# Kernel tuning notes

Measured on AMD Instinct MI355X. Metric: run time of the kernel, lower is better.

## Reference

```python
import jax, jax.numpy as jnp
import numpy as np

EPSILON = 1e-15
CUTOFF = 5.0
N_RBF = 16           # num_radial_filters -> RBF dim = 2*16+1 = 33
SCALE = 8            # _quadrature_points_per_atom_scaling


def poly_envelope_5_2(x):
    # e3nn.poly_envelope(5, 2): f'(x) ~ x^5 (1-x)^2, f(0)=1, f(1)=0
    x2 = x * x
    x6 = x2 * x2 * x2
    f = 1.0 - 28.0 * x6 + 48.0 * x6 * x - 21.0 * x6 * x2
    return jnp.where(x < 1.0, f, jnp.zeros_like(x))


def sin_cos_basis(r, n_rbf):
    r = r[..., None]                                  # [A,T,1]
    k = jnp.arange(1, n_rbf + 1, dtype=r.dtype)       # [n_rbf]
    return jnp.sqrt(2.0) * jnp.concatenate(
        [0.1 * jnp.ones_like(r), jnp.sin(k * jnp.pi * r), jnp.cos(k * jnp.pi * r)],
        axis=-1,
    )                                                 # [A,T,2*n_rbf+1]


def spherical_harmonics_l012_norm(d):
    # Real spherical harmonics up to l=2, e3nn m-ordering, normalization='norm'
    # (each l-block has unit norm for unit input directions).
    x, y, z = d[..., 0], d[..., 1], d[..., 2]
    r2 = x * x + y * y + z * z
    s3 = jnp.sqrt(3.0)
    one = jnp.ones_like(x)
    return jnp.stack(
        [
            one,                       # l=0
            y, z, x,                   # l=1 (m=-1,0,1)
            s3 * x * y,                # l=2 m=-2
            s3 * y * z,                # l=2 m=-1
            0.5 * (3.0 * z * z - r2),  # l=2 m=0
            s3 * x * z,                # l=2 m=1
            0.5 * s3 * (x * x - y * y) # l=2 m=2
        ],
        axis=-1,
    )                                  # [A,T,9]


def setup_inputs() -> dict:
    key = jax.random.key(0)
    k1, k2, k3, k4 = jax.random.split(key, 4)
    A, N = 64, 200000
    nuc_pos = 4.0 * jax.random.normal(k1, (A, 3), dtype=jnp.float32)
    grid_coords = 4.0 * jax.random.normal(k2, (N, 3), dtype=jnp.float32)
    weights = jax.random.uniform(k3, (N,), dtype=jnp.float32)
    n = jax.random.uniform(k4, (N,), dtype=jnp.float32)
    atom_mask = jnp.ones((A,), dtype=bool)
    return {"nuc_pos": nuc_pos, "atom_mask": atom_mask,
            "grid_coords": grid_coords, "weights": weights, "n": n}


def reference(nuc_pos, atom_mask, grid_coords, weights, n):
    g = grid_coords / CUTOFF                          # [N,3]
    p = nuc_pos / CUTOFF                              # [A,3]
    diff = p[:, None] - g[None]                       # [A,N,3]
    dist = jnp.linalg.norm(diff, axis=-1)             # [A,N]
    A, N = dist.shape
    T = min(N, SCALE * N // A)                        # static
    idx = jnp.argsort(dist, axis=1)[:, :T]            # [A,T] nearest grid points
    diff = jnp.take_along_axis(diff, idx[:, :, None], axis=1)   # [A,T,3]
    dist = jnp.take_along_axis(dist, idx, axis=1)                # [A,T]
    n_t = n[idx]                                      # [A,T]
    w_t = weights[idx]                                # [A,T]
    rbf = sin_cos_basis(dist, N_RBF) * poly_envelope_5_2(dist)[..., None]  # [A,T,33]
    dirs = diff / (dist[..., None] + EPSILON)         # [A,T,3]
    sh = spherical_harmonics_l012_norm(dirs)          # [A,T,9]
    node_feats = jnp.einsum('atr,ath,at,at->arh', rbf, sh, n_t, w_t)  # [A,33,9]
    return node_feats
```

## Files before the change

kernel.cpp:

```cpp
#include <hip/hip_runtime.h>
#include <hip/hip_fp16.h>


typedef float f32x4 __attribute__((ext_vector_type(4)));
typedef int   i32x4 __attribute__((ext_vector_type(4)));

#define SLICES 32
#define NB1    256
#define NB2    512
#define CLAMP0 4000u
#define NCHUNK SLICES
#define PBSTR  304
#define CUT25  0x41C80000u
#define WROWS  49
#define CSTR   136
#define CSTRD  (CSTR / 2)

__device__ __forceinline__ unsigned pack2h(float a, float b) {
  __half2 h = __floats2half2_rn(a, b);
  return *reinterpret_cast<unsigned*>(&h);
}

__device__ __forceinline__ unsigned pkbf(float a, float b) {
  unsigned r;
  asm("v_cvt_pk_bf16_f32 %0, %1, %2" : "=v"(r) : "v"(a), "v"(b));
  return r;
}

__device__ __forceinline__ void mfma_acc(f32x4& d, i32x4 a, i32x4 b) {
  asm("v_mfma_f32_16x16x32_bf16 %0, %1, %2, %0" : "+v"(d) : "v"(a), "v"(b));
}

__global__ __launch_bounds__(256) void enc_hist_store(
    const float* __restrict__ nuc, const float* __restrict__ grid,
    const float* __restrict__ wv, const float* __restrict__ nv, int N,
    unsigned* __restrict__ hists, unsigned* __restrict__ cnt,
    unsigned* __restrict__ bitsArr, uint2* __restrict__ pay, int scap,
    unsigned* __restrict__ ghist2) {
  __shared__ unsigned lh[4][NB1];
  __shared__ unsigned s_cnt;
  int a = blockIdx.x / SLICES, s = blockIdx.x % SLICES;
  int tid = threadIdx.x, lane = tid & 63, w = tid >> 6;
  if (tid < NB1) {
    lh[0][tid] = 0; lh[1][tid] = 0; lh[2][tid] = 0; lh[3][tid] = 0;
  }
  if (tid == 0) s_cnt = 0;
  {
    const int stripe = NB2 / SLICES;
    if (tid < stripe) ghist2[(size_t)a * NB2 + s * stripe + tid] = 0;
  }
  __syncthreads();
  unsigned* lhw = lh[w];

  float px = nuc[3*a+0], py = nuc[3*a+1], pz = nuc[3*a+2];
  unsigned* segb = bitsArr + (size_t)blockIdx.x * scap;
  uint2*    segp = pay     + (size_t)blockIdx.x * scap;
  const float4* G4 = (const float4*)grid;
  const float4* W4 = (const float4*)wv;
  const float4* V4 = (const float4*)nv;
  int nq = N >> 2;
  int qper = (nq + SLICES - 1) / SLICES;
  int qlo = s * qper, qhi = min(nq, qlo + qper);

  for (int qb = qlo; qb < qhi; qb += 256) {
    int qi = qb + tid;
    bool qv = qi < qhi;
    float dxs[4], dys[4], dzs[4], nws[4];
    unsigned bt[4];
    if (qv) {
      float4 A4 = G4[3*qi], B4 = G4[3*qi+1], C4 = G4[3*qi+2];
      float4 w4 = W4[qi], v4 = V4[qi];
      float xs[4] = {A4.x, A4.w, B4.z, C4.y};
      float ys[4] = {A4.y, B4.x, B4.w, C4.z};
      float zs[4] = {A4.z, B4.y, C4.x, C4.w};
      nws[0] = v4.x * w4.x; nws[1] = v4.y * w4.y;
      nws[2] = v4.z * w4.z; nws[3] = v4.w * w4.w;
      #pragma unroll
      for (int k = 0; k < 4; ++k) {
        float dx = px - xs[k], dy = py - ys[k], dz = pz - zs[k];
        dxs[k] = dx; dys[k] = dy; dzs[k] = dz;
        float d2 = __fmaf_rn(dx, dx, __fmaf_rn(dy, dy, __fmul_rn(dz, dz)));
        bt[k] = __float_as_uint(d2);
        if (bt[k] < CUT25) {
          int cb = (int)(bt[k] >> 18) - (int)CLAMP0;
          atomicAdd(&lhw[cb > 0 ? cb : 0], 1u);
        }
      }
    } else {
      #pragma unroll
      for (int k = 0; k < 4; ++k) bt[k] = 0xFFFFFFFFu;
    }
    unsigned csel = 0;
    #pragma unroll
    for (int k = 0; k < 4; ++k) csel += (bt[k] < CUT25) ? 1u : 0u;
    unsigned p = csel;
    #pragma unroll
    for (int d = 1; d < 64; d <<= 1) {
      unsigned t = __shfl_up(p, d);
      if (lane >= d) p += t;
    }
    unsigned wtot = __shfl(p, 63);
    unsigned excl = p - csel;
    unsigned base = 0;
    if (wtot) {
      if (lane == 0) base = atomicAdd(&s_cnt, wtot);
      base = __shfl(base, 0);
      unsigned pos = base + excl;
      #pragma unroll
      for (int k = 0; k < 4; ++k) {
        if (bt[k] < CUT25) {
          if (pos < (unsigned)scap) {
            segb[pos] = bt[k];
            segp[pos] = make_uint2(pack2h(dxs[k], dys[k]), pack2h(dzs[k], nws[k]));
          }
          ++pos;
        }
      }
    }
  }
  if (s == SLICES - 1) {
    for (int i = 4*nq + tid; i < N; i += 256) {
      float dx = px - grid[3*i+0], dy = py - grid[3*i+1], dz = pz - grid[3*i+2];
      float d2 = __fmaf_rn(dx, dx, __fmaf_rn(dy, dy, __fmul_rn(dz, dz)));
      unsigned bits = __float_as_uint(d2);
      bool sel = bits < CUT25;
      if (sel) {
        int cb = (int)(bits >> 18) - (int)CLAMP0;
        atomicAdd(&lhw[cb > 0 ? cb : 0], 1u);
      }
      unsigned long long mm = __ballot(sel);
      if (mm) {
        int leader = __ffsll(mm) - 1;
        unsigned base = 0;
        if (lane == leader) base = atomicAdd(&s_cnt, (unsigned)__popcll(mm));
        base = __shfl(base, leader);
        if (sel) {
          unsigned pos = base + (unsigned)__popcll(mm & ((1ull << lane) - 1ull));
          if (pos < (unsigned)scap) {
            segb[pos] = bits;
            segp[pos] = make_uint2(pack2h(dx, dy), pack2h(dz, nv[i] * wv[i]));
          }
        }
      }
    }
  }
  __syncthreads();
  if (tid < NB1) {
    unsigned v = lh[0][tid] + lh[1][tid] + lh[2][tid] + lh[3][tid];
    hists[(size_t)blockIdx.x * NB1 + tid] = v;
  }
  if (tid == 0) cnt[blockIdx.x] = s_cnt;
}

__global__ __launch_bounds__(256) void enc_scan1(
    const unsigned* __restrict__ hists, unsigned T,
    unsigned* __restrict__ b1r, unsigned* __restrict__ r2r) {
  __shared__ unsigned lh[NB1];
  __shared__ unsigned s_bin, s_pre;
  int a = blockIdx.x, tid = threadIdx.x;
  if (tid < NB1) {
    unsigned acc = 0;
    const unsigned* base = hists + (size_t)a * SLICES * NB1 + tid;
    #pragma unroll 8
    for (int t = 0; t < SLICES; ++t) acc += base[(size_t)t * NB1];
    lh[tid] = acc;
  }
  if (tid == 0) { s_bin = NB1 - 1; s_pre = 0; }
  __syncthreads();
  if (tid < 64) {
    int lane = tid, base = 4 * lane;
    unsigned h0 = lh[base], h1 = lh[base+1], h2 = lh[base+2], h3 = lh[base+3];
    unsigned ssum = h0 + h1 + h2 + h3;
    unsigned p = ssum;
    #pragma unroll
    for (int d = 1; d < 64; d <<= 1) {
      unsigned t = __shfl_up(p, d);
      if (lane >= d) p += t;
    }
    unsigned excl = p - ssum;
    if (excl < T && T <= p) {
      unsigned cum = excl;
      unsigned hh[4] = {h0, h1, h2, h3};
      #pragma unroll
      for (int k = 0; k < 4; ++k) {
        if (cum + hh[k] >= T) { s_bin = (unsigned)(base + k); s_pre = cum; break; }
        cum += hh[k];
      }
    }
  }
  __syncthreads();
  if (tid == 0) { b1r[a] = s_bin; r2r[a] = T - s_pre; }
}

__global__ __launch_bounds__(256) void enc_fine(
    const unsigned* __restrict__ b1r, const unsigned* __restrict__ cnt,
    const unsigned* __restrict__ bitsArr, int scap,
    unsigned* __restrict__ ghist2) {
  int seg_id = blockIdx.x;
  int a = seg_id / SLICES;
  unsigned b1c = b1r[a];
  unsigned tb1 = b1c + CLAMP0;
  int total = min((int)cnt[seg_id], scap);
  const unsigned* segb = bitsArr + (size_t)seg_id * scap;
  unsigned* gh2 = ghist2 + (size_t)a * NB2;
  for (int i = threadIdx.x; i < total; i += 256) {
    unsigned bits = segb[i];
    unsigned cb = bits >> 18;
    bool match = b1c ? (cb == tb1) : (cb <= CLAMP0);
    if (match) atomicAdd(&gh2[(bits >> 9) & (NB2 - 1)], 1u);
  }
}

__global__ __launch_bounds__(256) void enc_scan2(
    const unsigned* __restrict__ ghist2, const unsigned* __restrict__ b1r,
    const unsigned* __restrict__ r2r, unsigned* __restrict__ thr) {
  __shared__ unsigned lh2[NB2];
  __shared__ unsigned s_bin2;
  int a = blockIdx.x, tid = threadIdx.x;
  const unsigned* gh2 = ghist2 + (size_t)a * NB2;
  lh2[tid] = gh2[tid];
  lh2[tid + 256] = gh2[tid + 256];
  if (tid == 0) s_bin2 = NB2 - 1;
  __syncthreads();
  unsigned R = r2r[a];
  if (tid < 64) {
    int lane = tid, base = 8 * lane;
    unsigned hh[8], ssum = 0;
    #pragma unroll
    for (int k = 0; k < 8; ++k) { hh[k] = lh2[base + k]; ssum += hh[k]; }
    unsigned p = ssum;
    #pragma unroll
    for (int d = 1; d < 64; d <<= 1) {
      unsigned t = __shfl_up(p, d);
      if (lane >= d) p += t;
    }
    unsigned excl = p - ssum;
    if (excl < R && R <= p) {
      unsigned cum = excl;
      #pragma unroll
      for (int k = 0; k < 8; ++k) {
        if (cum + hh[k] >= R) { s_bin2 = (unsigned)(base + k); break; }
        cum += hh[k];
      }
    }
  }
  __syncthreads();
  if (tid == 0) thr[a] = ((b1r[a] + CLAMP0) << 9) | s_bin2;
}

__global__ __launch_bounds__(256, 3) void enc_accum(
    const unsigned* __restrict__ thrv, const unsigned* __restrict__ cnt,
    const unsigned* __restrict__ bitsArr, const uint2* __restrict__ pay,
    int scap, float* __restrict__ pb) {
  __shared__ __align__(16) unsigned short lds[4][WROWS * CSTR];
  int seg_id = blockIdx.x;
  int a = seg_id / SLICES;
  int tid = threadIdx.x, lane = tid & 63, w = tid >> 6;
  unsigned short* SB = &lds[w][0];
  unsigned* SBd = (unsigned*)SB;

  {
    i32x4 z = {0, 0, 0, 0};
    i32x4* zp = (i32x4*)SB;
    #pragma unroll
    for (int t = 0; t < 14; ++t) {
      int idx = lane + t * 64;
      if (idx < (WROWS * CSTR) / 8) zp[idx] = z;
    }
  }

  unsigned thr = thrv[a];
  int total = min((int)cnt[seg_id], scap);
  const unsigned* lstb = bitsArr + (size_t)seg_id * scap;
  const uint2*    lstp = pay     + (size_t)seg_id * scap;

  f32x4 acc0 = {0,0,0,0}, acc1 = {0,0,0,0}, acc2 = {0,0,0,0};
  int m = lane & 15, q = lane >> 4;
  const float SQRT2 = 1.41421356237309515f;
  const float PIF   = 3.14159265358979323846f;
  const float S3    = 1.73205080756887729f;

  int jp = w * 128 + 2 * lane;
  uint2 b2N = make_uint2(0xFFFFFFFFu, 0xFFFFFFFFu);
  uint4 p4N = make_uint4(0u, 0u, 0u, 0u);
  if (jp < total) {
    b2N = *reinterpret_cast<const uint2*>(&lstb[jp]);
    p4N = *reinterpret_cast<const uint4*>(&lstp[jp]);
  }

  for (int jb = w * 128; jb < total; jb += 512) {
    uint2 b2 = b2N; uint4 p4 = p4N;
    int jn = jb + 512 + 2 * lane;
    if (jn < total) {
      b2N = *reinterpret_cast<const uint2*>(&lstb[jn]);
      p4N = *reinterpret_cast<const uint4*>(&lstp[jn]);
    }
    int jj = jb + 2 * lane;
    bool live0 = (jj     < total) && ((b2.x >> 9) <= thr);
    bool live1 = (jj + 1 < total) && ((b2.y >> 9) <= thr);

    float d20 = live0 ? __uint_as_float(b2.x) : 1.0f;
    float d21 = live1 ? __uint_as_float(b2.y) : 1.0f;
    __half2 hxy0 = *reinterpret_cast<const __half2*>(&p4.x);
    __half2 hzn0 = *reinterpret_cast<const __half2*>(&p4.y);
    __half2 hxy1 = *reinterpret_cast<const __half2*>(&p4.z);
    __half2 hzn1 = *reinterpret_cast<const __half2*>(&p4.w);
    float dx0 = live0 ? __low2float(hxy0) : 0.f;
    float dy0 = live0 ? __high2float(hxy0) : 0.f;
    float dz0 = live0 ? __low2float(hzn0) : 0.f;
    float nw0 = live0 ? __high2float(hzn0) : 0.f;
    float dx1 = live1 ? __low2float(hxy1) : 0.f;
    float dy1 = live1 ? __high2float(hxy1) : 0.f;
    float dz1 = live1 ? __low2float(hzn1) : 0.f;
    float nw1 = live1 ? __high2float(hzn1) : 0.f;

#if __has_builtin(__builtin_amdgcn_sqrtf)
    float rn0 = __builtin_amdgcn_sqrtf(d20) * 0.2f;
    float rn1 = __builtin_amdgcn_sqrtf(d21) * 0.2f;
#else
    float rn0 = sqrtf(d20) * 0.2f;
    float rn1 = sqrtf(d21) * 0.2f;
#endif
    float x20 = rn0 * rn0, x21 = rn1 * rn1;
    float x60 = x20 * x20 * x20, x61 = x21 * x21 * x21;
    float e0 = __fmaf_rn(x60, __fmaf_rn(-21.f, x20, __fmaf_rn(48.f, rn0, -28.f)), 1.f);
    float e1 = __fmaf_rn(x61, __fmaf_rn(-21.f, x21, __fmaf_rn(48.f, rn1, -28.f)), 1.f);
    float f0 = live0 ? SQRT2 * e0 : 0.f;
    float f1 = live1 ? SQRT2 * e1 : 0.f;
#if __has_builtin(__builtin_amdgcn_rcpf)
    float inv0 = 0.2f * __builtin_amdgcn_rcpf(rn0 + 1e-15f);
    float inv1 = 0.2f * __builtin_amdgcn_rcpf(rn1 + 1e-15f);
#else
    float inv0 = 0.2f / (rn0 + 1e-15f);
    float inv1 = 0.2f / (rn1 + 1e-15f);
#endif
    float X0 = dx0 * inv0, Y0 = dy0 * inv0, Z0 = dz0 * inv0;
    float X1 = dx1 * inv1, Y1 = dy1 * inv1, Z1 = dz1 * inv1;
    float r20 = __fmaf_rn(X0, X0, __fmaf_rn(Y0, Y0, Z0 * Z0));
    float r21 = __fmaf_rn(X1, X1, __fmaf_rn(Y1, Y1, Z1 * Z1));

    SBd[(33+0)*CSTRD + lane] = pkbf(nw0,            nw1);
    SBd[(33+1)*CSTRD + lane] = pkbf(nw0 * Y0,       nw1 * Y1);
    SBd[(33+2)*CSTRD + lane] = pkbf(nw0 * Z0,       nw1 * Z1);
    SBd[(33+3)*CSTRD + lane] = pkbf(nw0 * X0,       nw1 * X1);
    SBd[(33+4)*CSTRD + lane] = pkbf(nw0 * S3*X0*Y0, nw1 * S3*X1*Y1);
    SBd[(33+5)*CSTRD + lane] = pkbf(nw0 * S3*Y0*Z0, nw1 * S3*Y1*Z1);
    SBd[(33+6)*CSTRD + lane] = pkbf(nw0 * 0.5f*__fmaf_rn(3.f, Z0*Z0, -r20),
                                    nw1 * 0.5f*__fmaf_rn(3.f, Z1*Z1, -r21));
    SBd[(33+7)*CSTRD + lane] = pkbf(nw0 * S3*X0*Z0, nw1 * S3*X1*Z1);
    SBd[(33+8)*CSTRD + lane] = pkbf(nw0 * 0.5f*S3*(X0*X0 - Y0*Y0),
                                    nw1 * 0.5f*S3*(X1*X1 - Y1*Y1));
    float s10, c10, s11, c11;
    __sincosf(PIF * rn0, &s10, &c10);
    __sincosf(PIF * rn1, &s11, &c11);
    SBd[0*CSTRD + lane]  = pkbf(0.1f * f0, 0.1f * f1);
    float sk0 = s10, ck0 = c10, sk1 = s11, ck1 = c11;
    SBd[1*CSTRD + lane]  = pkbf(f0 * sk0, f1 * sk1);
    SBd[17*CSTRD + lane] = pkbf(f0 * ck0, f1 * ck1);
    #pragma unroll
    for (int k = 2; k <= 16; ++k) {
      float sn0 = __fmaf_rn(sk0, c10, ck0 * s10);
      float cn0 = __fmaf_rn(ck0, c10, -(sk0 * s10));
      float sn1 = __fmaf_rn(sk1, c11, ck1 * s11);
      float cn1 = __fmaf_rn(ck1, c11, -(sk1 * s11));
      sk0 = sn0; ck0 = cn0; sk1 = sn1; ck1 = cn1;
      SBd[k*CSTRD + lane]      = pkbf(f0 * sk0, f1 * sk1);
      SBd[(16+k)*CSTRD + lane] = pkbf(f0 * ck0, f1 * ck1);
    }
    #pragma unroll
    for (int g = 0; g < 4; ++g) {
      int cb = 8 * q + 32 * g;
      i32x4 bf = *(const i32x4*)&SB[(33 + m) * CSTR + cb];
      i32x4 a0 = *(const i32x4*)&SB[(0  + m) * CSTR + cb];
      mfma_acc(acc0, a0, bf);
      i32x4 a1 = *(const i32x4*)&SB[(16 + m) * CSTR + cb];
      mfma_acc(acc1, a1, bf);
      i32x4 a2 = *(const i32x4*)&SB[(32 + m) * CSTR + cb];
      mfma_acc(acc2, a2, bf);
    }
  }
  asm volatile("s_nop 7\n\ts_nop 7" : "+v"(acc0), "+v"(acc1), "+v"(acc2));

  float* redw = (float*)&lds[w][0];
  if (m < 9) {
    #pragma unroll
    for (int t = 0; t < 4; ++t) {
      int row = 4 * q + t;
      redw[(row +  0) * 9 + m] = acc0[t];
      redw[(row + 16) * 9 + m] = acc1[t];
      if (row + 32 < 33) redw[(row + 32) * 9 + m] = acc2[t];
    }
  }
  __syncthreads();
  float* pbb = pb + (size_t)blockIdx.x * PBSTR;
  for (int v = tid; v < 297; v += 256) {
    float s0 = ((const float*)&lds[0][0])[v] + ((const float*)&lds[1][0])[v];
    float s1 = ((const float*)&lds[2][0])[v] + ((const float*)&lds[3][0])[v];
    pbb[v] = s0 + s1;
  }
}

__global__ __launch_bounds__(256) void enc_reduce(
    const float* __restrict__ pb, float* __restrict__ out, int nout) {
  int idx = blockIdx.x * 256 + threadIdx.x;
  if (idx >= nout) return;
  int a = idx / 297, v = idx - a * 297;
  const float* p = pb + (size_t)a * NCHUNK * PBSTR + v;
  float s = 0.f;
  #pragma unroll 8
  for (int k = 0; k < NCHUNK; ++k) s += p[(size_t)k * PBSTR];
  out[idx] = s;
}

extern "C" void kernel_launch(void* const* d_in, const int* in_sizes, int n_in,
                              void* d_out, int out_size, void* d_ws, size_t ws_size,
                              hipStream_t stream) {
  const float* nuc  = (const float*)d_in[0];
  const float* grid = (const float*)d_in[2];
  const float* wts  = (const float*)d_in[3];
  const float* nn   = (const float*)d_in[4];
  int A = in_sizes[0] / 3;
  int N = in_sizes[2] / 3;
  long long t8 = (8LL * (long long)N) / (long long)A;
  unsigned T = (unsigned)(t8 < (long long)N ? t8 : (long long)N);

  unsigned* ws      = (unsigned*)d_ws;
  unsigned* cnt     = ws;
  unsigned* b1r     = cnt + A * SLICES;
  unsigned* r2r     = b1r + A;
  unsigned* thr     = r2r + A;
  unsigned* hists   = thr + A;
  unsigned* ghist2  = hists + (size_t)A * SLICES * NB1;
  float*    pb      = (float*)(ghist2 + (size_t)A * NB2);
  unsigned* bitsArr = (unsigned*)(pb + (size_t)A * NCHUNK * PBSTR);

  int nq   = N >> 2;
  int qper = (nq + SLICES - 1) / SLICES;
  int SCAP = qper * 4 + 4;
  {
    long long head  = (long long)(bitsArr - ws);
    long long avail = (long long)(ws_size / 4) - head;
    long long need  = 3LL * SCAP * A * SLICES;
    if (avail > 0 && need > avail) SCAP = (int)(avail / (3LL * A * SLICES));
    SCAP &= ~1;
  }
  uint2* pay = (uint2*)(bitsArr + (size_t)A * SLICES * SCAP);
  float* out = (float*)d_out;
  int nout = A * 297;

  enc_hist_store<<<A * SLICES,         256, 0, stream>>>(nuc, grid, wts, nn, N, hists,
                                                         cnt, bitsArr, pay, SCAP, ghist2);
  enc_scan1     <<<A,                  256, 0, stream>>>(hists, T, b1r, r2r);
  enc_fine      <<<A * SLICES,         256, 0, stream>>>(b1r, cnt, bitsArr, SCAP, ghist2);
  enc_scan2     <<<A,                  256, 0, stream>>>(ghist2, b1r, r2r, thr);
  enc_accum     <<<A * SLICES,         256, 0, stream>>>(thr, cnt, bitsArr, pay, SCAP, pb);
  enc_reduce    <<<(nout + 255) / 256, 256, 0, stream>>>(pb, out, nout);
}
```

Measured before the change: 54.98 us.

## Fold per-atom scan kernels into fine-histogram and accumulate kernels

The two small per-atom scan kernels are removed. Every fine-histogram block now redundantly rebuilds its atom's coarse histogram from the per-slice histograms and finds the threshold bin itself. Every accumulate block recomputes the second-level scan from the global fine histogram in shared-memory scratch before zeroing it. This cuts two kernel launches and their serialization points, at the cost of 32x redundant histogram reads and scans per atom.

```diff
diff --git a/kernel.cpp b/kernel.cpp
--- a/kernel.cpp
+++ b/kernel.cpp
@@ -152,12 +152,16 @@
   if (tid == 0) cnt[blockIdx.x] = s_cnt;
 }
 
-__global__ __launch_bounds__(256) void enc_scan1(
-    const unsigned* __restrict__ hists, unsigned T,
-    unsigned* __restrict__ b1r, unsigned* __restrict__ r2r) {
+__global__ __launch_bounds__(256) void enc_fine(
+    const unsigned* __restrict__ hists, const unsigned* __restrict__ cnt,
+    const unsigned* __restrict__ bitsArr, int scap, unsigned T,
+    unsigned* __restrict__ b1r, unsigned* __restrict__ r2r,
+    unsigned* __restrict__ ghist2) {
   __shared__ unsigned lh[NB1];
   __shared__ unsigned s_bin, s_pre;
-  int a = blockIdx.x, tid = threadIdx.x;
+  int seg_id = blockIdx.x;
+  int a = seg_id / SLICES, s = seg_id % SLICES;
+  int tid = threadIdx.x;
   if (tid < NB1) {
     unsigned acc = 0;
     const unsigned* base = hists + (size_t)a * SLICES * NB1 + tid;
@@ -189,21 +193,14 @@
     }
   }
   __syncthreads();
-  if (tid == 0) { b1r[a] = s_bin; r2r[a] = T - s_pre; }
-}
-
-__global__ __launch_bounds__(256) void enc_fine(
-    const unsigned* __restrict__ b1r, const unsigned* __restrict__ cnt,
-    const unsigned* __restrict__ bitsArr, int scap,
-    unsigned* __restrict__ ghist2) {
-  int seg_id = blockIdx.x;
-  int a = seg_id / SLICES;
-  unsigned b1c = b1r[a];
+  unsigned b1c = s_bin;
+  if (s == 0 && tid == 0) { b1r[a] = s_bin; r2r[a] = T - s_pre; }
+
   unsigned tb1 = b1c + CLAMP0;
   int total = min((int)cnt[seg_id], scap);
   const unsigned* segb = bitsArr + (size_t)seg_id * scap;
   unsigned* gh2 = ghist2 + (size_t)a * NB2;
-  for (int i = threadIdx.x; i < total; i += 256) {
+  for (int i = tid; i < total; i += 256) {
     unsigned bits = segb[i];
     unsigned cb = bits >> 18;
     bool match = b1c ? (cb == tb1) : (cb <= CLAMP0);
@@ -211,48 +208,13 @@
   }
 }
 
-__global__ __launch_bounds__(256) void enc_scan2(
-    const unsigned* __restrict__ ghist2, const unsigned* __restrict__ b1r,
-    const unsigned* __restrict__ r2r, unsigned* __restrict__ thr) {
-  __shared__ unsigned lh2[NB2];
-  __shared__ unsigned s_bin2;
-  int a = blockIdx.x, tid = threadIdx.x;
-  const unsigned* gh2 = ghist2 + (size_t)a * NB2;
-  lh2[tid] = gh2[tid];
-  lh2[tid + 256] = gh2[tid + 256];
-  if (tid == 0) s_bin2 = NB2 - 1;
-  __syncthreads();
-  unsigned R = r2r[a];
-  if (tid < 64) {
-    int lane = tid, base = 8 * lane;
-    unsigned hh[8], ssum = 0;
-    #pragma unroll
-    for (int k = 0; k < 8; ++k) { hh[k] = lh2[base + k]; ssum += hh[k]; }
-    unsigned p = ssum;
-    #pragma unroll
-    for (int d = 1; d < 64; d <<= 1) {
-      unsigned t = __shfl_up(p, d);
-      if (lane >= d) p += t;
-    }
-    unsigned excl = p - ssum;
-    if (excl < R && R <= p) {
-      unsigned cum = excl;
-      #pragma unroll
-      for (int k = 0; k < 8; ++k) {
-        if (cum + hh[k] >= R) { s_bin2 = (unsigned)(base + k); break; }
-        cum += hh[k];
-      }
-    }
-  }
-  __syncthreads();
-  if (tid == 0) thr[a] = ((b1r[a] + CLAMP0) << 9) | s_bin2;
-}
-
 __global__ __launch_bounds__(256, 3) void enc_accum(
-    const unsigned* __restrict__ thrv, const unsigned* __restrict__ cnt,
+    const unsigned* __restrict__ b1r, const unsigned* __restrict__ r2r,
+    const unsigned* __restrict__ ghist2, const unsigned* __restrict__ cnt,
     const unsigned* __restrict__ bitsArr, const uint2* __restrict__ pay,
     int scap, float* __restrict__ pb) {
   __shared__ __align__(16) unsigned short lds[4][WROWS * CSTR];
+  __shared__ unsigned s_bin2;
   int seg_id = blockIdx.x;
   int a = seg_id / SLICES;
   int tid = threadIdx.x, lane = tid & 63, w = tid >> 6;
@@ -260,6 +222,39 @@
   unsigned* SBd = (unsigned*)SB;
 
   {
+    unsigned* scratch = (unsigned*)&lds[0][0];
+    const unsigned* gh2 = ghist2 + (size_t)a * NB2;
+    scratch[tid] = gh2[tid];
+    scratch[tid + 256] = gh2[tid + 256];
+    if (tid == 0) s_bin2 = NB2 - 1;
+    __syncthreads();
+    unsigned R = r2r[a];
+    if (tid < 64) {
+      int lane2 = tid, base = 8 * lane2;
+      unsigned hh[8], ssum = 0;
+      #pragma unroll
+      for (int k = 0; k < 8; ++k) { hh[k] = scratch[base + k]; ssum += hh[k]; }
+      unsigned p = ssum;
+      #pragma unroll
+      for (int d = 1; d < 64; d <<= 1) {
+        unsigned t = __shfl_up(p, d);
+        if (lane2 >= d) p += t;
+      }
+      unsigned excl = p - ssum;
+      if (excl < R && R <= p) {
+        unsigned cum = excl;
+        #pragma unroll
+        for (int k = 0; k < 8; ++k) {
+          if (cum + hh[k] >= R) { s_bin2 = (unsigned)(base + k); break; }
+          cum += hh[k];
+        }
+      }
+    }
+    __syncthreads();
+  }
+  unsigned thr = ((b1r[a] + CLAMP0) << 9) | s_bin2;
+
+  {
     i32x4 z = {0, 0, 0, 0};
     i32x4* zp = (i32x4*)SB;
     #pragma unroll
@@ -269,7 +264,6 @@
     }
   }
 
-  unsigned thr = thrv[a];
   int total = min((int)cnt[seg_id], scap);
   const unsigned* lstb = bitsArr + (size_t)seg_id * scap;
   const uint2*    lstp = pay     + (size_t)seg_id * scap;
@@ -450,9 +444,9 @@
 
   enc_hist_store<<<A * SLICES,         256, 0, stream>>>(nuc, grid, wts, nn, N, hists,
                                                          cnt, bitsArr, pay, SCAP, ghist2);
-  enc_scan1     <<<A,                  256, 0, stream>>>(hists, T, b1r, r2r);
-  enc_fine      <<<A * SLICES,         256, 0, stream>>>(b1r, cnt, bitsArr, SCAP, ghist2);
-  enc_scan2     <<<A,                  256, 0, stream>>>(ghist2, b1r, r2r, thr);
-  enc_accum     <<<A * SLICES,         256, 0, stream>>>(thr, cnt, bitsArr, pay, SCAP, pb);
+  enc_fine      <<<A * SLICES,         256, 0, stream>>>(hists, cnt, bitsArr, SCAP, T,
+                                                         b1r, r2r, ghist2);
+  enc_accum     <<<A * SLICES,         256, 0, stream>>>(b1r, r2r, ghist2, cnt,
+                                                         bitsArr, pay, SCAP, pb);
   enc_reduce    <<<(nout + 255) / 256, 256, 0, stream>>>(pb, out, nout);
 }
```

Result: slower. 56.33 us (+2.5%).
